# Optimization experiments

Measured on AMD Instinct MI355X. Metric: run time of the kernel, lower is better.

Reference implementation:

```python
import jax, jax.numpy as jnp
import numpy as np

B, L, D_IN, D_EXP, N_EXP = 4, 2048, 1024, 1024, 8


def setup_inputs() -> dict:
    key = jax.random.key(0)
    ks = jax.random.split(key, 5)
    s_in = 1.0 / np.sqrt(D_IN)
    x = jax.random.normal(ks[0], (B, L, D_IN), dtype=jnp.float32)
    # per-expert Dense kernels/biases: (n, d_in, d_exp), (n, d_exp)
    We = jax.random.normal(ks[1], (N_EXP, D_IN, D_EXP), dtype=jnp.float32) * s_in
    be = jnp.zeros((N_EXP, D_EXP), dtype=jnp.float32)
    # gating Dense: (d_in, n), (n)
    Wg = jax.random.normal(ks[2], (D_IN, N_EXP), dtype=jnp.float32) * s_in
    bg = jnp.zeros((N_EXP,), dtype=jnp.float32)
    return {"x": x, "We": We, "be": be, "Wg": Wg, "bg": bg}


def reference(x, We, be, Wg, bg):
    # expert outputs: (b, l, n, d_exp) = relu(x @ We[n] + be[n])
    h = jax.nn.relu(jnp.einsum('bld,ndk->blnk', x, We) + be[None, None, :, :])
    # gate: softmax over experts, (b, l, n)
    gate = jax.nn.softmax(jnp.einsum('bld,dn->bln', x, Wg) + bg, axis=-1)
    # gated weighted sum over experts -> (b, l, d_exp)
    return jnp.einsum('bln,blnk->blk', gate, h)
```

## Files before the change

kernel.cpp:

```cpp
#include <hip/hip_runtime.h>
#include <hip/hip_bf16.h>
#include <stdint.h>

#define M_TOT 8192
#define DIN   1024
#define DEXP  1024
#define NEXP  8

#define BM 256
#define BN 128
#define BK 32
#define NT 128
#define KPP 32
#define SLOT_E 16384
#define EXPSZ (DEXP * DIN)

typedef __attribute__((ext_vector_type(8))) short bf16x8;
typedef __attribute__((ext_vector_type(16))) float f32x16;
typedef __attribute__((ext_vector_type(8))) unsigned short us8;

typedef __attribute__((address_space(1))) void* as1vp;
typedef __attribute__((address_space(3))) void* as3vp;

__device__ __forceinline__ unsigned short f2bf(float f) {
    union { float f; unsigned u; } v; v.f = f;
    return (unsigned short)((v.u + 0x7fffu + ((v.u >> 16) & 1u)) >> 16);
}

__device__ __forceinline__ void gl_lds16(const unsigned short* g, unsigned short* l) {
    __builtin_amdgcn_global_load_lds((as1vp)g, (as3vp)l, 16, 0, 0);
}

#define MFMA32(va, vb, vc) __builtin_amdgcn_mfma_f32_32x32x16_bf16(va, vb, vc, 0, 0, 0)

__global__ __launch_bounds__(256) void cvt_x_k(const float* __restrict__ in,
                                               unsigned short* __restrict__ out, int n8) {
    int i = blockIdx.x * 256 + threadIdx.x;
    int stride = gridDim.x * 256;
    for (; i < n8; i += stride) {
        const float4* p = (const float4*)in + (size_t)i * 2;
        float4 a = p[0], b = p[1];
        us8 o;
        o[0] = f2bf(a.x); o[1] = f2bf(a.y); o[2] = f2bf(a.z); o[3] = f2bf(a.w);
        o[4] = f2bf(b.x); o[5] = f2bf(b.y); o[6] = f2bf(b.z); o[7] = f2bf(b.w);
        *(us8*)(out + (size_t)i * 8) = o;
    }
}

__global__ __launch_bounds__(256) void cvt_w_k(const float* __restrict__ We,
                                               unsigned short* __restrict__ Wt) {
    __shared__ float tile[64][65];
    int n  = blockIdx.z;
    int k0 = blockIdx.y * 64;
    int j0 = blockIdx.x * 64;
    int t  = threadIdx.x;
    int tr = t >> 6, tc = t & 63;
    const float* src = We + (size_t)n * DIN * DEXP;
    #pragma unroll
    for (int rr = 0; rr < 16; ++rr) {
        int r = rr * 4 + tr;
        tile[r][tc] = src[(size_t)(k0 + r) * DEXP + j0 + tc];
    }
    __syncthreads();
    unsigned short* dst = Wt + (size_t)n * DEXP * DIN;
    #pragma unroll
    for (int rr = 0; rr < 16; ++rr) {
        int r = rr * 4 + tr;
        dst[(size_t)(j0 + r) * DIN + k0 + tc] = f2bf(tile[tc][r]);
    }
}

__global__ __launch_bounds__(256) void gate_k(const float* __restrict__ x,
                                              const float* __restrict__ Wg,
                                              const float* __restrict__ bg,
                                              float* __restrict__ gate) {
    __shared__ float wgt[NEXP][DIN];
    int t = threadIdx.x;
    for (int idx = t; idx < DIN * NEXP; idx += 256)
        wgt[idx & 7][idx >> 3] = Wg[idx];
    __syncthreads();
    int wid = t >> 6, lane = t & 63;
    for (int m = blockIdx.x * 4 + wid; m < M_TOT; m += gridDim.x * 4) {
        const float* xr = x + (size_t)m * DIN;
        float acc[NEXP];
        #pragma unroll
        for (int n = 0; n < NEXP; ++n) acc[n] = 0.f;
        for (int i = 0; i < DIN / 64; ++i) {
            int d = i * 64 + lane;
            float xv = xr[d];
            #pragma unroll
            for (int n = 0; n < NEXP; ++n) acc[n] = fmaf(xv, wgt[n][d], acc[n]);
        }
        #pragma unroll
        for (int n = 0; n < NEXP; ++n) {
            #pragma unroll
            for (int off = 32; off; off >>= 1) acc[n] += __shfl_xor(acc[n], off);
            acc[n] += bg[n];
        }
        float mx = acc[0];
        #pragma unroll
        for (int n = 1; n < NEXP; ++n) mx = fmaxf(mx, acc[n]);
        float s = 0.f, e[NEXP];
        #pragma unroll
        for (int n = 0; n < NEXP; ++n) { e[n] = __expf(acc[n] - mx); s += e[n]; }
        float inv = 1.f / s;
        if (lane < NEXP) gate[(size_t)m * NEXP + lane] = e[lane] * inv;
    }
}

__global__ __launch_bounds__(512, 2) void moe_k(const unsigned short* __restrict__ Xb,
                                                const unsigned short* __restrict__ Wt,
                                                const float* __restrict__ gate,
                                                const float* __restrict__ be,
                                                float* __restrict__ out) {
    __shared__ __align__(16) unsigned short lds[3 * SLOT_E];
    __shared__ float gateL[BM * NEXP];
    __shared__ float biasL[NEXP * BN];

    const int t    = threadIdx.x;
    const int lane = t & 63;
    const int wv   = t >> 6;
    const int wm   = wv >> 1;
    const int wn   = wv & 1;
    const int l31  = lane & 31;
    const int lhi  = lane >> 5;

    const int b    = blockIdx.x;
    const int lg   = (b & 7) * 32 + (b >> 3);
    const int brow = (lg >> 3) * BM;
    const int bcol = (lg & 7) * BN;

    const int sA = (t >> 2) * DIN + ((((t & 3) - (t >> 3)) & 3) * 8);
    const unsigned short* gA = Xb + (size_t)brow * DIN;
    const unsigned short* gB = Wt + (size_t)bcol * DIN;

    const int kc0 = ((lhi + (l31 >> 1)) & 3) * 8;
    const int kc1 = kc0 ^ 16;
    const int aBase = (wm * 64 + l31) * 32;
    const int bBase = 8192 + (wn * 64 + l31) * 32;

#define STAGE_A(sl_, k0_) do { \
    const unsigned short* g_ = gA + (k0_) + sA; \
    unsigned short* d_ = (unsigned short*)lds + (sl_) * SLOT_E + t * 8; \
    gl_lds16(g_, d_); gl_lds16(g_ + 128 * DIN, d_ + 4096); } while (0)
#define STAGE_B0(sl_, e_, k0_) do { \
    gl_lds16(gB + (size_t)(e_) * EXPSZ + (k0_) + sA, \
             (unsigned short*)lds + (sl_) * SLOT_E + 8192 + t * 8); } while (0)
#define STAGE_B1(sl_, e_, k0_) do { \
    gl_lds16(gB + (size_t)(e_) * EXPSZ + (k0_) + sA, \
             (unsigned short*)lds + (sl_) * SLOT_E + 12288 + t * 8); } while (0)

    f32x16 acc_e0[2][2] = {};
    f32x16 acc_e1[2][2] = {};
    f32x16 acc_o[2][2]  = {};

    {
        const float* gp = gate + (size_t)brow * NEXP;
        ((float4*)gateL)[t] = ((const float4*)gp)[t];
        if (t < 256)
            ((float4*)biasL)[t] =
                *(const float4*)(be + (size_t)(t >> 5) * DEXP + bcol + (t & 31) * 4);
    }
    STAGE_A(0, 0);  STAGE_B0(0, 0, 0);  STAGE_B1(0, 1, 0);
    STAGE_A(1, 32); STAGE_B0(1, 0, 32); STAGE_B1(1, 1, 32);
    asm volatile("s_waitcnt vmcnt(4)" ::: "memory");
    asm volatile("s_waitcnt lgkmcnt(0)" ::: "memory");
    __builtin_amdgcn_s_barrier();

    int sl = 0, sl2 = 2;
    for (int T = 0; T < NT; ++T) {
        const unsigned short* L = lds + sl * SLOT_E;
        const int p2  = (T + 2) >> 5;
        const int k2  = ((T + 2) & (KPP - 1)) * BK;
        const bool doSt = (T < NT - 2);

        bf16x8 a[2][2], b0[2][2], b1[2][2];

        #pragma unroll
        for (int mf = 0; mf < 2; ++mf) {
            a[mf][0] = *(const bf16x8*)(L + aBase + mf * 1024 + kc0);
            a[mf][1] = *(const bf16x8*)(L + aBase + mf * 1024 + kc1);
        }
        #pragma unroll
        for (int nf = 0; nf < 2; ++nf) {
            b0[nf][0] = *(const bf16x8*)(L + bBase + nf * 1024 + kc0);
            b0[nf][1] = *(const bf16x8*)(L + bBase + nf * 1024 + kc1);
        }
        if (doSt) STAGE_A(sl2, k2);
        __builtin_amdgcn_s_barrier();
        asm volatile("s_waitcnt lgkmcnt(0)" ::: "memory");
        __builtin_amdgcn_sched_barrier(0);
        __builtin_amdgcn_s_setprio(1);
        #pragma unroll
        for (int mf = 0; mf < 2; ++mf)
            #pragma unroll
            for (int nf = 0; nf < 2; ++nf) {
                acc_e0[mf][nf] = MFMA32(a[mf][0], b0[nf][0], acc_e0[mf][nf]);
                acc_e0[mf][nf] = MFMA32(a[mf][1], b0[nf][1], acc_e0[mf][nf]);
            }
        __builtin_amdgcn_s_setprio(0);
        __builtin_amdgcn_s_barrier();

        #pragma unroll
        for (int nf = 0; nf < 2; ++nf) {
            b1[nf][0] = *(const bf16x8*)(L + bBase + 4096 + nf * 1024 + kc0);
            b1[nf][1] = *(const bf16x8*)(L + bBase + 4096 + nf * 1024 + kc1);
        }
        if (doSt) {
            STAGE_B0(sl2, p2 * 2, k2);
            STAGE_B1(sl2, p2 * 2 + 1, k2);
            asm volatile("s_waitcnt vmcnt(4)" ::: "memory");
        } else {
            asm volatile("s_waitcnt vmcnt(0)" ::: "memory");
        }
        __builtin_amdgcn_s_barrier();
        asm volatile("s_waitcnt lgkmcnt(0)" ::: "memory");
        __builtin_amdgcn_sched_barrier(0);
        __builtin_amdgcn_s_setprio(1);
        #pragma unroll
        for (int mf = 0; mf < 2; ++mf)
            #pragma unroll
            for (int nf = 0; nf < 2; ++nf) {
                acc_e1[mf][nf] = MFMA32(a[mf][0], b1[nf][0], acc_e1[mf][nf]);
                acc_e1[mf][nf] = MFMA32(a[mf][1], b1[nf][1], acc_e1[mf][nf]);
            }
        __builtin_amdgcn_s_setprio(0);
        __builtin_amdgcn_s_barrier();

        if ((T & (KPP - 1)) == (KPP - 1)) {
            const int e0 = (T >> 5) * 2, e1 = e0 + 1;
            float bi0[2], bi1[2];
            #pragma unroll
            for (int nf = 0; nf < 2; ++nf) {
                bi0[nf] = biasL[e0 * BN + wn * 64 + nf * 32 + l31];
                bi1[nf] = biasL[e1 * BN + wn * 64 + nf * 32 + l31];
            }
            #pragma unroll
            for (int mf = 0; mf < 2; ++mf) {
                #pragma unroll
                for (int reg = 0; reg < 16; ++reg) {
                    const int rl = wm * 64 + mf * 32 + (reg & 3) + 8 * (reg >> 2) + 4 * lhi;
                    const float g0 = gateL[rl * NEXP + e0];
                    const float g1 = gateL[rl * NEXP + e1];
                    #pragma unroll
                    for (int nf = 0; nf < 2; ++nf) {
                        acc_o[mf][nf][reg] += g0 * fmaxf(acc_e0[mf][nf][reg] + bi0[nf], 0.f)
                                            + g1 * fmaxf(acc_e1[mf][nf][reg] + bi1[nf], 0.f);
                    }
                }
            }
            #pragma unroll
            for (int mf = 0; mf < 2; ++mf)
                #pragma unroll
                for (int nf = 0; nf < 2; ++nf) {
                    acc_e0[mf][nf] = (f32x16){};
                    acc_e1[mf][nf] = (f32x16){};
                }
        }

        sl  = (sl  == 2) ? 0 : sl  + 1;
        sl2 = (sl2 == 2) ? 0 : sl2 + 1;
    }

    #pragma unroll
    for (int mf = 0; mf < 2; ++mf) {
        #pragma unroll
        for (int reg = 0; reg < 16; ++reg) {
            const int rl = wm * 64 + mf * 32 + (reg & 3) + 8 * (reg >> 2) + 4 * lhi;
            float* op = out + (size_t)(brow + rl) * DEXP + bcol + wn * 64 + l31;
            #pragma unroll
            for (int nf = 0; nf < 2; ++nf) op[nf * 32] = acc_o[mf][nf][reg];
        }
    }
#undef STAGE_A
#undef STAGE_B0
#undef STAGE_B1
}

extern "C" void kernel_launch(void* const* d_in, const int* in_sizes, int n_in,
                              void* d_out, int out_size, void* d_ws, size_t ws_size,
                              hipStream_t stream) {
    const float* x  = (const float*)d_in[0];
    const float* We = (const float*)d_in[1];
    const float* be = (const float*)d_in[2];
    const float* Wg = (const float*)d_in[3];
    const float* bg = (const float*)d_in[4];
    float* out = (float*)d_out;

    unsigned short* Xb = (unsigned short*)d_ws;
    unsigned short* Wt = Xb + (size_t)M_TOT * DIN;
    float* gate = (float*)(Wt + (size_t)NEXP * DEXP * DIN);

    hipLaunchKernelGGL(cvt_x_k, dim3(2048), dim3(256), 0, stream, x, Xb, M_TOT * DIN / 8);
    hipLaunchKernelGGL(cvt_w_k, dim3(16, 16, 8), dim3(256), 0, stream, We, Wt);
    hipLaunchKernelGGL(gate_k, dim3(512), dim3(256), 0, stream, x, Wg, bg, gate);
    hipLaunchKernelGGL(moe_k, dim3((M_TOT / BM) * (DEXP / BN)), dim3(512), 0, stream,
                       Xb, Wt, gate, be, out);
}
```

Measured before the change: 171.9 us.

## Deepen LDS pipeline to four stages and prefetch next-tile fragments into registers

Grows the shared-memory ring from three to four slots and issues global-to-LDS loads three tiles ahead. The A/B0/B1 fragments for the next K-tile are read into registers while the current tile's MFMAs run, with partial lgkmcnt waits. This cuts the workgroup barriers per iteration from four to one, reducing synchronisation stalls between load and compute phases. The cost is more LDS use (about 140KB per block) and longer register lifetimes for the prefetched fragments, which may raise register pressure.

```diff
diff --git a/kernel.cpp b/kernel.cpp
--- a/kernel.cpp
+++ b/kernel.cpp
@@ -113,7 +113,7 @@
                                                 const float* __restrict__ gate,
                                                 const float* __restrict__ be,
                                                 float* __restrict__ out) {
-    __shared__ __align__(16) unsigned short lds[3 * SLOT_E];
+    __shared__ __align__(16) unsigned short lds[4 * SLOT_E];
     __shared__ float gateL[BM * NEXP];
     __shared__ float biasL[NEXP * BN];
 
@@ -136,8 +136,10 @@
 
     const int kc0 = ((lhi + (l31 >> 1)) & 3) * 8;
     const int kc1 = kc0 ^ 16;
-    const int aBase = (wm * 64 + l31) * 32;
-    const int bBase = 8192 + (wn * 64 + l31) * 32;
+    const int aOff0 = (wm * 64 + l31) * 32 + kc0;
+    const int aOff1 = (wm * 64 + l31) * 32 + kc1;
+    const int bOff0 = 8192 + (wn * 64 + l31) * 32 + kc0;
+    const int bOff1 = 8192 + (wn * 64 + l31) * 32 + kc1;
 
 #define STAGE_A(sl_, k0_) do { \
     const unsigned short* g_ = gA + (k0_) + sA; \
@@ -150,9 +152,26 @@
     gl_lds16(gB + (size_t)(e_) * EXPSZ + (k0_) + sA, \
              (unsigned short*)lds + (sl_) * SLOT_E + 12288 + t * 8); } while (0)
 
+#define RD_B0(L_) do { \
+    b0[0][0] = *(const bf16x8*)((L_) + bOff0); \
+    b0[0][1] = *(const bf16x8*)((L_) + bOff1); \
+    b0[1][0] = *(const bf16x8*)((L_) + bOff0 + 1024); \
+    b0[1][1] = *(const bf16x8*)((L_) + bOff1 + 1024); } while (0)
+#define RD_A(L_) do { \
+    a[0][0] = *(const bf16x8*)((L_) + aOff0); \
+    a[0][1] = *(const bf16x8*)((L_) + aOff1); \
+    a[1][0] = *(const bf16x8*)((L_) + aOff0 + 1024); \
+    a[1][1] = *(const bf16x8*)((L_) + aOff1 + 1024); } while (0)
+#define RD_B1(L_) do { \
+    b1[0][0] = *(const bf16x8*)((L_) + bOff0 + 4096); \
+    b1[0][1] = *(const bf16x8*)((L_) + bOff1 + 4096); \
+    b1[1][0] = *(const bf16x8*)((L_) + bOff0 + 5120); \
+    b1[1][1] = *(const bf16x8*)((L_) + bOff1 + 5120); } while (0)
+
     f32x16 acc_e0[2][2] = {};
     f32x16 acc_e1[2][2] = {};
     f32x16 acc_o[2][2]  = {};
+    bf16x8 a[2][2], b0[2][2], b1[2][2];
 
     {
         const float* gp = gate + (size_t)brow * NEXP;
@@ -163,32 +182,17 @@
     }
     STAGE_A(0, 0);  STAGE_B0(0, 0, 0);  STAGE_B1(0, 1, 0);
     STAGE_A(1, 32); STAGE_B0(1, 0, 32); STAGE_B1(1, 1, 32);
+    STAGE_A(2, 64); STAGE_B0(2, 0, 64); STAGE_B1(2, 1, 64);
     asm volatile("s_waitcnt vmcnt(4)" ::: "memory");
     asm volatile("s_waitcnt lgkmcnt(0)" ::: "memory");
     __builtin_amdgcn_s_barrier();
-
-    int sl = 0, sl2 = 2;
+    RD_B0(lds); RD_A(lds);
+    __builtin_amdgcn_sched_barrier(0);
+    RD_B1(lds);
+    __builtin_amdgcn_sched_barrier(0);
+
     for (int T = 0; T < NT; ++T) {
-        const unsigned short* L = lds + sl * SLOT_E;
-        const int p2  = (T + 2) >> 5;
-        const int k2  = ((T + 2) & (KPP - 1)) * BK;
-        const bool doSt = (T < NT - 2);
-
-        bf16x8 a[2][2], b0[2][2], b1[2][2];
-
-        #pragma unroll
-        for (int mf = 0; mf < 2; ++mf) {
-            a[mf][0] = *(const bf16x8*)(L + aBase + mf * 1024 + kc0);
-            a[mf][1] = *(const bf16x8*)(L + aBase + mf * 1024 + kc1);
-        }
-        #pragma unroll
-        for (int nf = 0; nf < 2; ++nf) {
-            b0[nf][0] = *(const bf16x8*)(L + bBase + nf * 1024 + kc0);
-            b0[nf][1] = *(const bf16x8*)(L + bBase + nf * 1024 + kc1);
-        }
-        if (doSt) STAGE_A(sl2, k2);
-        __builtin_amdgcn_s_barrier();
-        asm volatile("s_waitcnt lgkmcnt(0)" ::: "memory");
+        asm volatile("s_waitcnt lgkmcnt(4)" ::: "memory");
         __builtin_amdgcn_sched_barrier(0);
         __builtin_amdgcn_s_setprio(1);
         #pragma unroll
@@ -199,22 +203,14 @@
                 acc_e0[mf][nf] = MFMA32(a[mf][1], b0[nf][1], acc_e0[mf][nf]);
             }
         __builtin_amdgcn_s_setprio(0);
-        __builtin_amdgcn_s_barrier();
-
-        #pragma unroll
-        for (int nf = 0; nf < 2; ++nf) {
-            b1[nf][0] = *(const bf16x8*)(L + bBase + 4096 + nf * 1024 + kc0);
-            b1[nf][1] = *(const bf16x8*)(L + bBase + 4096 + nf * 1024 + kc1);
-        }
-        if (doSt) {
-            STAGE_B0(sl2, p2 * 2, k2);
-            STAGE_B1(sl2, p2 * 2 + 1, k2);
-            asm volatile("s_waitcnt vmcnt(4)" ::: "memory");
+
+        if (T < NT - 1) {
+            const unsigned short* L1 = lds + ((T + 1) & 3) * SLOT_E;
+            RD_B0(L1);
+            asm volatile("s_waitcnt lgkmcnt(4)" ::: "memory");
         } else {
-            asm volatile("s_waitcnt vmcnt(0)" ::: "memory");
-        }
-        __builtin_amdgcn_s_barrier();
-        asm volatile("s_waitcnt lgkmcnt(0)" ::: "memory");
+            asm volatile("s_waitcnt lgkmcnt(0)" ::: "memory");
+        }
         __builtin_amdgcn_sched_barrier(0);
         __builtin_amdgcn_s_setprio(1);
         #pragma unroll
@@ -225,7 +221,6 @@
                 acc_e1[mf][nf] = MFMA32(a[mf][1], b1[nf][1], acc_e1[mf][nf]);
             }
         __builtin_amdgcn_s_setprio(0);
-        __builtin_amdgcn_s_barrier();
 
         if ((T & (KPP - 1)) == (KPP - 1)) {
             const int e0 = (T >> 5) * 2, e1 = e0 + 1;
@@ -258,8 +253,24 @@
                 }
         }
 
-        sl  = (sl  == 2) ? 0 : sl  + 1;
-        sl2 = (sl2 == 2) ? 0 : sl2 + 1;
+        if (T < NT - 1) {
+            const unsigned short* L1 = lds + ((T + 1) & 3) * SLOT_E;
+            RD_A(L1);
+            __builtin_amdgcn_sched_barrier(0);
+            RD_B1(L1);
+            __builtin_amdgcn_sched_barrier(0);
+        }
+
+        if (T < NT - 3) {
+            const int s3 = (T + 3) & 3;
+            const int e3 = ((T + 3) >> 5) * 2;
+            const int k3 = ((T + 3) & (KPP - 1)) * BK;
+            STAGE_A(s3, k3); STAGE_B0(s3, e3, k3); STAGE_B1(s3, e3 + 1, k3);
+            asm volatile("s_waitcnt vmcnt(4)" ::: "memory");
+        } else {
+            asm volatile("s_waitcnt vmcnt(0)" ::: "memory");
+        }
+        __builtin_amdgcn_s_barrier();
     }
 
     #pragma unroll
@@ -275,6 +286,9 @@
 #undef STAGE_A
 #undef STAGE_B0
 #undef STAGE_B1
+#undef RD_A
+#undef RD_B0
+#undef RD_B1
 }
 
 extern "C" void kernel_launch(void* const* d_in, const int* in_sizes, int n_in,
```

New measurement: 159.8 us. 1.08x faster.
